# Kernel tuning notes

Hardware: AMD Instinct MI355X
Metric: run time of the kernel (lower is better)

## Reference

```python
import jax, jax.numpy as jnp
import numpy as np

T, B, I, H, L = 128, 64, 1024, 1024, 8


def setup_inputs() -> dict:
    key = jax.random.key(0)
    k0, k1, k2, k3, k4 = jax.random.split(key, 5)
    w_scale = 1.0 / np.sqrt(H)
    return {
        "inputs": jax.random.normal(k0, (T, B, I), dtype=jnp.float32),
        "Wih": jax.random.normal(k1, (L, 4, I, H), dtype=jnp.float32) * w_scale,
        "Whh": jax.random.normal(k2, (L, 4, H, H), dtype=jnp.float32) * w_scale,
        "bih": jax.random.normal(k3, (L, 4, H), dtype=jnp.float32),
        "bhh": jax.random.normal(k4, (L, 4, H), dtype=jnp.float32),
    }


def reference(inputs, Wih, Whh, bih, bhh):
    L_ = Wih.shape[0]
    B_ = inputs.shape[1]
    H_ = Wih.shape[-1]
    bias = bih + bhh  # [L,4,H]
    c0 = jnp.zeros((L_, B_, H_), dtype=inputs.dtype)
    h0 = jnp.zeros((L_, B_, H_), dtype=inputs.dtype)

    def step(carry, x_t):
        c, h = carry  # each [L,B,H]
        cur = x_t  # [B,I]
        cs, hs = [], []
        for j in range(L_):
            # gates: [4,B,H]
            gates = (jnp.einsum('bi,gih->gbh', cur, Wih[j])
                     + jnp.einsum('bk,gkh->gbh', h[j], Whh[j])
                     + bias[j][:, None, :])
            ig = jax.nn.sigmoid(gates[0])
            fg = jax.nn.sigmoid(gates[1])
            cg = jnp.tanh(gates[2])
            og = jax.nn.sigmoid(gates[3])
            cj = fg * c[j] + ig * cg
            hj = og * jnp.tanh(cj)
            cs.append(cj)
            hs.append(hj)
            cur = hj
        return (jnp.stack(cs), jnp.stack(hs)), None

    (c_fin, h_fin), _ = jax.lax.scan(step, (c0, h0), inputs)
    return h_fin[-1]  # [B,H] hidden state of last layer
```

## Files before the change

kernel.cpp:

```cpp
#include <hip/hip_runtime.h>


typedef __attribute__((ext_vector_type(8))) short short8;
typedef __attribute__((ext_vector_type(4))) float f32x4;

#define T_ 128
#define B_ 64
#define H_ 1024
#define L_ 8

__device__ __forceinline__ unsigned short f2bf(float f) {
    unsigned u = __builtin_bit_cast(unsigned, f);
    u += 0x7fff + ((u >> 16) & 1);
    return (unsigned short)(u >> 16);
}

__global__ void pack_weights(const float* __restrict__ Wih, const float* __restrict__ Whh,
                             unsigned short* __restrict__ packedW) {
    int tid = blockIdx.x * 256 + threadIdx.x;
    int lane = tid & 63;
    int kchunk = (tid >> 6) & 63;
    int ntile = (tid >> 12) & 255;
    int l = tid >> 20;
    int n = ntile * 16 + (lane & 15);
    int g = n >> 10;
    int h = n & 1023;
    int kbase = kchunk * 32 + ((lane >> 4) << 3);
    short8 v;
#pragma unroll
    for (int j = 0; j < 8; ++j) {
        int k = kbase + j;
        float w = (k < 1024) ? Wih[(((l * 4 + g) * 1024 + k) << 10) + h]
                             : Whh[(((l * 4 + g) * 1024 + (k - 1024)) << 10) + h];
        v[j] = (short)f2bf(w);
    }
    *(short8*)(packedW + (size_t)tid * 8) = v;
}

__global__ void prep_misc(const float* __restrict__ x, const float* __restrict__ bih,
                          const float* __restrict__ bhh, unsigned short* __restrict__ xbf,
                          float* __restrict__ bias, float* __restrict__ c_state,
                          unsigned short* __restrict__ h_buf) {
    int tid = blockIdx.x * 256 + threadIdx.x;
    xbf[tid] = f2bf(x[tid]);
    if (tid < L_ * 4096) bias[tid] = bih[tid] + bhh[tid];
    if (tid < L_ * B_ * H_) c_state[tid] = 0.f;
    if (tid < 2 * L_ * B_ * H_) h_buf[tid] = 0;
}

__global__ __launch_bounds__(256, 2)
void lstm_diag(const unsigned short* __restrict__ packedW,
               const unsigned short* __restrict__ xbf,
               const float* __restrict__ bias,
               float* __restrict__ c_state,
               unsigned short* __restrict__ h_buf,
               float* __restrict__ out,
               int d, int lmin) {
    __shared__ __align__(16) unsigned short Abuf[64 * 264];
    const int l = lmin + blockIdx.y;
    const int t = d - l;
    const int tid = threadIdx.x;
    const int lane = tid & 63;
    const int g = tid >> 6;
    const int u0 = blockIdx.x * 32;
    const int m = lane & 15;
    const int q = lane >> 4;

    const unsigned short* xsrc = (l == 0) ? (xbf + t * (B_ * H_))
                                          : (h_buf + ((t & 1) * L_ + (l - 1)) * (B_ * H_));
    const unsigned short* hsrc = h_buf + (((t + 1) & 1) * L_ + l) * (B_ * H_);

    f32x4 acc[4][2];
#pragma unroll
    for (int mt = 0; mt < 4; ++mt) { acc[mt][0] = (f32x4)0.f; acc[mt][1] = (f32x4)0.f; }

    const int ntile0 = g * 64 + (u0 >> 4);
    const unsigned short* bbase0 = packedW + (((size_t)l * 256 + ntile0) * 32768 + lane * 8);
    const unsigned short* bbase1 = bbase0 + 32768;

    for (int kb = 0; kb < 8; ++kb) {
        __syncthreads();
        const unsigned short* src = (kb < 4) ? (xsrc + kb * 256) : (hsrc + (kb - 4) * 256);
#pragma unroll
        for (int p = 0; p < 8; ++p) {
            int idx = p * 256 + tid;
            int row = idx >> 5;
            int seg = idx & 31;
            short8 v = *(const short8*)(src + row * 1024 + seg * 8);
            *(short8*)(&Abuf[row * 264 + seg * 8]) = v;
        }
        __syncthreads();
#pragma unroll
        for (int c = 0; c < 8; ++c) {
            short8 afr[4];
#pragma unroll
            for (int mt = 0; mt < 4; ++mt)
                afr[mt] = *(const short8*)(&Abuf[(mt * 16 + m) * 264 + c * 32 + q * 8]);
            int kc = kb * 8 + c;
            short8 b0 = *(const short8*)(bbase0 + (size_t)kc * 512);
            short8 b1 = *(const short8*)(bbase1 + (size_t)kc * 512);
#pragma unroll
            for (int mt = 0; mt < 4; ++mt) {
                acc[mt][0] = __builtin_amdgcn_mfma_f32_16x16x32_bf16(afr[mt], b0, acc[mt][0], 0, 0, 0);
                acc[mt][1] = __builtin_amdgcn_mfma_f32_16x16x32_bf16(afr[mt], b1, acc[mt][1], 0, 0, 0);
            }
        }
    }

    __syncthreads();
    float* Gbuf = (float*)Abuf;
#pragma unroll
    for (int mt = 0; mt < 4; ++mt)
#pragma unroll
        for (int nt = 0; nt < 2; ++nt)
#pragma unroll
            for (int r = 0; r < 4; ++r) {
                int b = mt * 16 + q * 4 + r;
                int u = nt * 16 + m;
                Gbuf[(g * 64 + b) * 33 + u] = acc[mt][nt][r];
            }
    __syncthreads();

#pragma unroll
    for (int it = 0; it < 8; ++it) {
        int idx = it * 256 + tid;
        int b = idx >> 5;
        int u = idx & 31;
        int nb = u0 + u;
        float gi = Gbuf[(0 * 64 + b) * 33 + u] + bias[l * 4096 + nb];
        float gf = Gbuf[(1 * 64 + b) * 33 + u] + bias[l * 4096 + 1024 + nb];
        float gc = Gbuf[(2 * 64 + b) * 33 + u] + bias[l * 4096 + 2048 + nb];
        float go = Gbuf[(3 * 64 + b) * 33 + u] + bias[l * 4096 + 3072 + nb];
        float ig = 1.f / (1.f + __expf(-gi));
        float fg = 1.f / (1.f + __expf(-gf));
        float cg = tanhf(gc);
        float og = 1.f / (1.f + __expf(-go));
        int cidx = (l * B_ + b) * H_ + nb;
        float cnew = fg * c_state[cidx] + ig * cg;
        c_state[cidx] = cnew;
        float hnew = og * tanhf(cnew);
        h_buf[((t & 1) * L_ + l) * (B_ * H_) + b * H_ + nb] = f2bf(hnew);
        if (l == 7 && t == 127) out[b * H_ + nb] = hnew;
    }
}

extern "C" void kernel_launch(void* const* d_in, const int* in_sizes, int n_in,
                              void* d_out, int out_size, void* d_ws, size_t ws_size,
                              hipStream_t stream) {
    const float* x   = (const float*)d_in[0];
    const float* Wih = (const float*)d_in[1];
    const float* Whh = (const float*)d_in[2];
    const float* bih = (const float*)d_in[3];
    const float* bhh = (const float*)d_in[4];
    float* out = (float*)d_out;

    char* ws = (char*)d_ws;
    unsigned short* packedW = (unsigned short*)ws;
    unsigned short* xbf     = (unsigned short*)(ws + 134217728);
    float* bias             = (float*)(ws + 134217728 + 16777216);
    float* c_state          = (float*)(ws + 134217728 + 16777216 + 131072);
    unsigned short* h_buf   = (unsigned short*)(ws + 134217728 + 16777216 + 131072 + 2097152);

    hipLaunchKernelGGL(pack_weights, dim3(32768), dim3(256), 0, stream, Wih, Whh, packedW);
    hipLaunchKernelGGL(prep_misc, dim3(32768), dim3(256), 0, stream,
                       x, bih, bhh, xbf, bias, c_state, h_buf);
    for (int d = 0; d <= 134; ++d) {
        int lmin = d > 127 ? d - 127 : 0;
        int lmax = d < 7 ? d : 7;
        hipLaunchKernelGGL(lstm_diag, dim3(32, lmax - lmin + 1), dim3(256), 0, stream,
                           packedW, xbf, bias, c_state, h_buf, out, d, lmin);
    }
}
```

Before: 4.709 ms.

## Store activations in MFMA fragment layout and read A operands directly from global

Activations (x and h) are now stored pre-swizzled in the MFMA A-fragment layout, so each wave loads its operands straight from global/L2 with coalesced 16-byte loads. This removes the LDS staging and the per-k-block syncthreads. Each block now covers 16 hidden units instead of 32, which doubles the grid to 64 strips per layer and gives more parallelism on the small per-diagonal launches. The cost is that every block re-reads the full activation matrix from cache, the LDS reuse across the two n-tiles is lost, and only half the threads run the pointwise epilogue.

```diff
diff --git a/kernel.cpp b/kernel.cpp
--- a/kernel.cpp
+++ b/kernel.cpp
@@ -8,6 +8,7 @@
 #define B_ 64
 #define H_ 1024
 #define L_ 8
+#define SLAB 65536
 
 __device__ __forceinline__ unsigned short f2bf(float f) {
     unsigned u = __builtin_bit_cast(unsigned, f);
@@ -38,109 +39,115 @@
 }
 
 __global__ void prep_misc(const float* __restrict__ x, const float* __restrict__ bih,
-                          const float* __restrict__ bhh, unsigned short* __restrict__ xbf,
+                          const float* __restrict__ bhh, unsigned short* __restrict__ xA,
                           float* __restrict__ bias, float* __restrict__ c_state,
-                          unsigned short* __restrict__ h_buf) {
+                          unsigned short* __restrict__ hA) {
     int tid = blockIdx.x * 256 + threadIdx.x;
-    xbf[tid] = f2bf(x[tid]);
+    int ioct = tid & 127;
+    int b = (tid >> 7) & 63;
+    int t = tid >> 13;
+    int i0 = ioct * 8;
+    const float* src = x + ((size_t)(t * 64 + b) << 10) + i0;
+    short8 v;
+#pragma unroll
+    for (int j = 0; j < 8; ++j) v[j] = (short)f2bf(src[j]);
+    int kc = i0 >> 5;
+    int q = (i0 >> 3) & 3;
+    int mt = b >> 4;
+    int m = b & 15;
+    *(short8*)(xA + (size_t)t * SLAB + (((kc * 4 + mt) * 64 + q * 16 + m) << 3)) = v;
+
     if (tid < L_ * 4096) bias[tid] = bih[tid] + bhh[tid];
-    if (tid < L_ * B_ * H_) c_state[tid] = 0.f;
-    if (tid < 2 * L_ * B_ * H_) h_buf[tid] = 0;
+    if (tid < L_ * B_ * H_ / 2) { c_state[2 * tid] = 0.f; c_state[2 * tid + 1] = 0.f; }
+    if (tid < 131072) *(short8*)(hA + (size_t)tid * 8) = (short8)0;
 }
 
-__global__ __launch_bounds__(256, 2)
+__global__ __launch_bounds__(256)
 void lstm_diag(const unsigned short* __restrict__ packedW,
-               const unsigned short* __restrict__ xbf,
+               const unsigned short* __restrict__ xA,
                const float* __restrict__ bias,
                float* __restrict__ c_state,
-               unsigned short* __restrict__ h_buf,
+               unsigned short* __restrict__ hA,
                float* __restrict__ out,
                int d, int lmin) {
-    __shared__ __align__(16) unsigned short Abuf[64 * 264];
+    __shared__ float Gbuf[4 * 64 * 17];
     const int l = lmin + blockIdx.y;
     const int t = d - l;
+    const int strip = blockIdx.x;
     const int tid = threadIdx.x;
     const int lane = tid & 63;
     const int g = tid >> 6;
-    const int u0 = blockIdx.x * 32;
     const int m = lane & 15;
     const int q = lane >> 4;
 
-    const unsigned short* xsrc = (l == 0) ? (xbf + t * (B_ * H_))
-                                          : (h_buf + ((t & 1) * L_ + (l - 1)) * (B_ * H_));
-    const unsigned short* hsrc = h_buf + (((t + 1) & 1) * L_ + l) * (B_ * H_);
+    const unsigned short* A0 = (l == 0) ? (xA + (size_t)t * SLAB)
+                                        : (hA + (size_t)((t & 1) * L_ + (l - 1)) * SLAB);
+    const unsigned short* A1 = hA + (size_t)(((t + 1) & 1) * L_ + l) * SLAB;
+    const unsigned short* Bp = packedW
+        + ((size_t)l * 256 + g * 64 + strip) * 32768 + lane * 8;
 
-    f32x4 acc[4][2];
+    f32x4 acc[4];
 #pragma unroll
-    for (int mt = 0; mt < 4; ++mt) { acc[mt][0] = (f32x4)0.f; acc[mt][1] = (f32x4)0.f; }
+    for (int mt = 0; mt < 4; ++mt) acc[mt] = (f32x4)0.f;
 
-    const int ntile0 = g * 64 + (u0 >> 4);
-    const unsigned short* bbase0 = packedW + (((size_t)l * 256 + ntile0) * 32768 + lane * 8);
-    const unsigned short* bbase1 = bbase0 + 32768;
-
-    for (int kb = 0; kb < 8; ++kb) {
-        __syncthreads();
-        const unsigned short* src = (kb < 4) ? (xsrc + kb * 256) : (hsrc + (kb - 4) * 256);
+#pragma unroll 8
+    for (int kc = 0; kc < 32; ++kc) {
+        short8 bfr = *(const short8*)(Bp + kc * 512);
+        short8 a[4];
 #pragma unroll
-        for (int p = 0; p < 8; ++p) {
-            int idx = p * 256 + tid;
-            int row = idx >> 5;
-            int seg = idx & 31;
-            short8 v = *(const short8*)(src + row * 1024 + seg * 8);
-            *(short8*)(&Abuf[row * 264 + seg * 8]) = v;
-        }
-        __syncthreads();
+        for (int mt = 0; mt < 4; ++mt)
+            a[mt] = *(const short8*)(A0 + (((kc * 4 + mt) * 64 + lane) << 3));
 #pragma unroll
-        for (int c = 0; c < 8; ++c) {
-            short8 afr[4];
+        for (int mt = 0; mt < 4; ++mt)
+            acc[mt] = __builtin_amdgcn_mfma_f32_16x16x32_bf16(a[mt], bfr, acc[mt], 0, 0, 0);
+    }
+#pragma unroll 8
+    for (int kc = 0; kc < 32; ++kc) {
+        short8 bfr = *(const short8*)(Bp + (kc + 32) * 512);
+        short8 a[4];
 #pragma unroll
-            for (int mt = 0; mt < 4; ++mt)
-                afr[mt] = *(const short8*)(&Abuf[(mt * 16 + m) * 264 + c * 32 + q * 8]);
-            int kc = kb * 8 + c;
-            short8 b0 = *(const short8*)(bbase0 + (size_t)kc * 512);
-            short8 b1 = *(const short8*)(bbase1 + (size_t)kc * 512);
+        for (int mt = 0; mt < 4; ++mt)
+            a[mt] = *(const short8*)(A1 + (((kc * 4 + mt) * 64 + lane) << 3));
 #pragma unroll
-            for (int mt = 0; mt < 4; ++mt) {
-                acc[mt][0] = __builtin_amdgcn_mfma_f32_16x16x32_bf16(afr[mt], b0, acc[mt][0], 0, 0, 0);
-                acc[mt][1] = __builtin_amdgcn_mfma_f32_16x16x32_bf16(afr[mt], b1, acc[mt][1], 0, 0, 0);
-            }
-        }
+        for (int mt = 0; mt < 4; ++mt)
+            acc[mt] = __builtin_amdgcn_mfma_f32_16x16x32_bf16(a[mt], bfr, acc[mt], 0, 0, 0);
     }
 
-    __syncthreads();
-    float* Gbuf = (float*)Abuf;
 #pragma unroll
     for (int mt = 0; mt < 4; ++mt)
 #pragma unroll
-        for (int nt = 0; nt < 2; ++nt)
-#pragma unroll
-            for (int r = 0; r < 4; ++r) {
-                int b = mt * 16 + q * 4 + r;
-                int u = nt * 16 + m;
-                Gbuf[(g * 64 + b) * 33 + u] = acc[mt][nt][r];
-            }
+        for (int r = 0; r < 4; ++r)
+            Gbuf[(g * 64 + mt * 16 + q * 4 + r) * 17 + m] = acc[mt][r];
     __syncthreads();
 
+    if (tid < 128) {
+        int b = tid >> 1;
+        int oct = tid & 1;
+        int uH0 = strip * 16 + oct * 8;
+        const float* bs = bias + l * 4096;
+        float* cp = c_state + ((l * 64 + b) << 10) + uH0;
+        int kcH = uH0 >> 5, qH = (uH0 >> 3) & 3;
+        unsigned short* hp = hA + (size_t)((t & 1) * L_ + l) * SLAB
+                           + (((kcH * 4 + (b >> 4)) * 64 + qH * 16 + (b & 15)) << 3);
+        short8 hv;
 #pragma unroll
-    for (int it = 0; it < 8; ++it) {
-        int idx = it * 256 + tid;
-        int b = idx >> 5;
-        int u = idx & 31;
-        int nb = u0 + u;
-        float gi = Gbuf[(0 * 64 + b) * 33 + u] + bias[l * 4096 + nb];
-        float gf = Gbuf[(1 * 64 + b) * 33 + u] + bias[l * 4096 + 1024 + nb];
-        float gc = Gbuf[(2 * 64 + b) * 33 + u] + bias[l * 4096 + 2048 + nb];
-        float go = Gbuf[(3 * 64 + b) * 33 + u] + bias[l * 4096 + 3072 + nb];
-        float ig = 1.f / (1.f + __expf(-gi));
-        float fg = 1.f / (1.f + __expf(-gf));
-        float cg = tanhf(gc);
-        float og = 1.f / (1.f + __expf(-go));
-        int cidx = (l * B_ + b) * H_ + nb;
-        float cnew = fg * c_state[cidx] + ig * cg;
-        c_state[cidx] = cnew;
-        float hnew = og * tanhf(cnew);
-        h_buf[((t & 1) * L_ + l) * (B_ * H_) + b * H_ + nb] = f2bf(hnew);
-        if (l == 7 && t == 127) out[b * H_ + nb] = hnew;
+        for (int j = 0; j < 8; ++j) {
+            int ul = oct * 8 + j;
+            float gi = Gbuf[(0 * 64 + b) * 17 + ul] + bs[uH0 + j];
+            float gf = Gbuf[(1 * 64 + b) * 17 + ul] + bs[1024 + uH0 + j];
+            float gc = Gbuf[(2 * 64 + b) * 17 + ul] + bs[2048 + uH0 + j];
+            float go = Gbuf[(3 * 64 + b) * 17 + ul] + bs[3072 + uH0 + j];
+            float ig = 1.f / (1.f + __expf(-gi));
+            float fg = 1.f / (1.f + __expf(-gf));
+            float cg = tanhf(gc);
+            float og = 1.f / (1.f + __expf(-go));
+            float cnew = fg * cp[j] + ig * cg;
+            cp[j] = cnew;
+            float hnew = og * tanhf(cnew);
+            hv[j] = (short)f2bf(hnew);
+            if (l == 7 && t == 127) out[(b << 10) + uH0 + j] = hnew;
+        }
+        *(short8*)hp = hv;
     }
 }
 
@@ -156,18 +163,18 @@
 
     char* ws = (char*)d_ws;
     unsigned short* packedW = (unsigned short*)ws;
-    unsigned short* xbf     = (unsigned short*)(ws + 134217728);
+    unsigned short* xA      = (unsigned short*)(ws + 134217728);
     float* bias             = (float*)(ws + 134217728 + 16777216);
     float* c_state          = (float*)(ws + 134217728 + 16777216 + 131072);
-    unsigned short* h_buf   = (unsigned short*)(ws + 134217728 + 16777216 + 131072 + 2097152);
+    unsigned short* hA      = (unsigned short*)(ws + 134217728 + 16777216 + 131072 + 2097152);
 
     hipLaunchKernelGGL(pack_weights, dim3(32768), dim3(256), 0, stream, Wih, Whh, packedW);
-    hipLaunchKernelGGL(prep_misc, dim3(32768), dim3(256), 0, stream,
-                       x, bih, bhh, xbf, bias, c_state, h_buf);
+    hipLaunchKernelGGL(prep_misc, dim3(4096), dim3(256), 0, stream,
+                       x, bih, bhh, xA, bias, c_state, hA);
     for (int d = 0; d <= 134; ++d) {
         int lmin = d > 127 ? d - 127 : 0;
         int lmax = d < 7 ? d : 7;
-        hipLaunchKernelGGL(lstm_diag, dim3(32, lmax - lmin + 1), dim3(256), 0, stream,
-                           packedW, xbf, bias, c_state, h_buf, out, d, lmin);
+        hipLaunchKernelGGL(lstm_diag, dim3(64, lmax - lmin + 1), dim3(256), 0, stream,
+                           packedW, xA, bias, c_state, hA, out, d, lmin);
     }
 }
```

Result: slower. 6.104 ms (+29.6%).
